# Kernel optimization log

Hardware: AMD Instinct MI355X
Metric: run time of the kernel (lower is better)

The kernel has to match this reference:

```python
import jax, jax.numpy as jnp
import numpy as np

B, L, D, H, NE, M, NP, C, F2 = 2, 1024, 768, 12, 42, 8, 1722, 97, 256


def setup_inputs() -> dict:
    key = jax.random.key(0)
    ks = jax.random.split(key, 12)
    s = 0.02
    sequence_output = jax.random.normal(ks[0], (B, L, D), jnp.float32)
    attention = jax.random.uniform(ks[1], (B, H, L, L), jnp.float32)
    mention_idx = jax.random.randint(ks[2], (B, NE, M), 0, L)
    mention_mask = jax.random.randint(ks[3], (B, NE, M), 0, 2).at[:, :, 0].set(1)
    hts = jax.random.randint(ks[4], (B, NP, 2), 0, NE)
    return dict(
        sequence_output=sequence_output, attention=attention,
        mention_idx=mention_idx, mention_mask=mention_mask, hts=hts,
        W_lin=jax.random.normal(ks[5], (D, 3)) * s, b_lin=jnp.zeros((3,)),
        W_seg=jax.random.normal(ks[6], (3, F2)) * s, b_seg=jnp.zeros((F2,)),
        W_head=jax.random.normal(ks[7], (D, F2)) * s, b_head=jnp.zeros((F2,)),
        W_tail=jax.random.normal(ks[8], (D, F2)) * s, b_tail=jnp.zeros((F2,)),
        W_bil=jax.random.normal(ks[9], (C, F2, F2)) * s, b_bil=jnp.zeros((C,)),
    )


def reference(sequence_output, attention, mention_idx, mention_mask, hts,
              W_lin, b_lin, W_seg, b_seg, W_head, b_head, W_tail, b_tail,
              W_bil, b_bil):
    b_, l_, d_ = sequence_output.shape
    h_ = attention.shape[1]
    ne, m_ = mention_idx.shape[1:]
    NEG = jnp.asarray(-1e30, sequence_output.dtype)
    msk = mention_mask.astype(sequence_output.dtype)  # [B,NE,M]

    bidx = jnp.arange(b_)[:, None, None]
    # --- get_hrt: per-entity mention gather + logsumexp pool / mean pool ---
    ment_emb = sequence_output[bidx, mention_idx]              # [B,NE,M,D]
    ent_emb = jax.nn.logsumexp(jnp.where(msk[..., None] > 0, ment_emb, NEG), axis=2)  # [B,NE,D]
    ment_att = attention[bidx, :, mention_idx]                 # [B,NE,M,H,L]
    ent_att = (ment_att * msk[..., None, None]).sum(2) / msk.sum(2)[..., None, None]  # [B,NE,H,L]

    b2 = jnp.arange(b_)[:, None]
    hs = ent_emb[b2, hts[..., 0]]                              # [B,NP,D]
    ts = ent_emb[b2, hts[..., 1]]

    # --- get_channel_map: all ne*ne pair attention-weighted context ---
    hi = jnp.repeat(jnp.arange(ne), ne)
    ti = jnp.tile(jnp.arange(ne), ne)
    h_att = ent_att[:, hi]                                     # [B,NE*NE,H,L]
    t_att = ent_att[:, ti]
    ht_att = jnp.einsum('bphl,bphl->bpl', h_att, t_att) / h_   # mean over heads
    ht_att = ht_att / (ht_att.sum(-1, keepdims=True) + 1e-5)
    rs = jnp.einsum('bld,bpl->bpd', sequence_output, ht_att)   # [B,NE*NE,D]
    feature_map = rs.reshape(b_, ne, ne, d_)

    # self.linear (D->3) then segmentation net (stand-in: 1x1 conv 3->F2 + relu)
    attn_input = feature_map @ W_lin + b_lin                   # [B,NE,NE,3]
    attn_map = jax.nn.relu(attn_input @ W_seg + b_seg)         # [B,NE,NE,F2]

    # --- get_ht: gather pair features ---
    h_t = attn_map[b2, hts[..., 0], hts[..., 1]]               # [B,NP,F2]
    hs = jnp.tanh(hs @ W_head + b_head + h_t)
    ts = jnp.tanh(ts @ W_tail + b_tail + h_t)
    logits = jnp.einsum('bpi,oij,bpj->bpo', hs, W_bil, ts) + b_bil
    return logits.reshape(-1, logits.shape[-1])               # [B*NP, C]
```

## Files before the change

kernel.cpp:

```cpp
#include <hip/hip_runtime.h>
#include <hip/hip_bf16.h>
#include <math.h>

constexpr int BB = 2;
constexpr int LL = 1024;
constexpr int DD = 768;
constexpr int HH = 12;
constexpr int NEz = 42;
constexpr int MM = 8;
constexpr int NPp = 1722;
constexpr int CC = 97;
constexpr int FF = 256;
constexpr int PAIRS = NEz * NEz;
constexpr int TOTAL = BB * NPp;
constexpr int MTv = 256;
constexpr int NTt = 14;
constexpr int PADR = 3584;
constexpr int NOGv = 36;
constexpr int NWGv = NTt * NOGv;

typedef float f32x4 __attribute__((ext_vector_type(4)));
typedef short bf16x8 __attribute__((ext_vector_type(8)));
typedef unsigned int u32x2 __attribute__((ext_vector_type(2)));

__device__ inline short f2bs(float x) {
    __hip_bfloat16 b = __float2bfloat16(x);
    return *(short*)&b;
}
__device__ inline void gload16(const void* g, void* l) {
    __builtin_amdgcn_global_load_lds((const __attribute__((address_space(1))) unsigned int*)g,
                                     (__attribute__((address_space(3))) unsigned int*)l, 16, 0, 0);
}

__global__ void k_ent_emb(const float* __restrict__ seq, const int* __restrict__ midx,
                          const int* __restrict__ mmask, float* __restrict__ ent_emb) {
    int be = blockIdx.x;
    int b = be / NEz;
    int tid = threadIdx.x;
    int idx[MM], msk[MM];
#pragma unroll
    for (int m = 0; m < MM; ++m) {
        idx[m] = midx[be * MM + m];
        msk[m] = mmask[be * MM + m];
    }
    const float* sb = seq + (size_t)b * LL * DD;
    for (int d = tid; d < DD; d += 256) {
        float v[MM];
        float mx = -1e30f;
#pragma unroll
        for (int m = 0; m < MM; ++m) {
            v[m] = msk[m] ? sb[(size_t)idx[m] * DD + d] : -1e30f;
            mx = fmaxf(mx, v[m]);
        }
        float s = 0.f;
#pragma unroll
        for (int m = 0; m < MM; ++m) s += expf(v[m] - mx);
        ent_emb[(size_t)be * DD + d] = mx + logf(s);
    }
}

__global__ void k_ent_att(const float* __restrict__ att, const int* __restrict__ midx,
                          const int* __restrict__ mmask, float* __restrict__ ea) {
    int beh = blockIdx.x;
    int h = beh % HH;
    int be = beh / HH;
    int b = be / NEz;
    int tid = threadIdx.x;
    int idx[MM], msk[MM];
    float msum = 0.f;
#pragma unroll
    for (int m = 0; m < MM; ++m) {
        idx[m] = midx[be * MM + m];
        msk[m] = mmask[be * MM + m];
        msum += (float)msk[m];
    }
    float inv = 1.f / msum;
    const float* ab = att + ((size_t)b * HH + h) * LL * LL;
#pragma unroll
    for (int li = 0; li < 4; ++li) {
        int l = tid + li * 256;
        float acc = 0.f;
#pragma unroll
        for (int m = 0; m < MM; ++m)
            if (msk[m]) acc += ab[(size_t)idx[m] * LL + l];
        ea[(size_t)beh * LL + l] = acc * inv;
    }
}

__global__ void k_pairAB(const float* __restrict__ ea, const float* __restrict__ seq,
                         const float* __restrict__ Wl, float* __restrict__ szp) {
    int lcb = blockIdx.x;
    int b = blockIdx.y;
    int l0 = lcb * 8;
    int tid = threadIdx.x;
    int lane = tid & 63;
    int e1 = (tid >> 6) * 8 + (lane >> 3);
    int l = lane & 7;

    __shared__ float S[NEz][HH][9];
    __shared__ float sw[8][3];
    __shared__ float swp[24][17];

    for (int idx = tid; idx < NEz * HH * 8; idx += 384) {
        int e = idx / 96, rem = idx % 96;
        int h = rem / 8, ll = rem % 8;
        S[e][h][ll] = ea[((size_t)(b * NEz + e) * HH + h) * LL + l0 + ll];
    }
    {
        int cpair = tid % 24, s = tid / 24;
        if (s < 16) {
            int ll = cpair / 3, kk = cpair % 3;
            const float* sr = seq + ((size_t)b * LL + l0 + ll) * DD;
            float p = 0.f;
            for (int d = s * 48; d < s * 48 + 48; ++d) p += sr[d] * Wl[d * 3 + kk];
            swp[cpair][s] = p;
        }
    }
    __syncthreads();
    if (tid < 24) {
        float s = 0.f;
#pragma unroll
        for (int i = 0; i < 16; ++i) s += swp[tid][i];
        sw[tid / 3][tid % 3] = s;
    }
    __syncthreads();

    bool act = e1 < NEz;
    float e1r[HH];
#pragma unroll
    for (int h = 0; h < HH; ++h) e1r[h] = act ? S[e1][h][l] : 0.f;
    float sw0 = sw[l][0], sw1 = sw[l][1], sw2 = sw[l][2];

    for (int e2 = 0; e2 < NEz; ++e2) {
        float ht = 0.f;
#pragma unroll
        for (int h = 0; h < HH; ++h) ht += e1r[h] * S[e2][h][l];
        ht *= (1.0f / HH);
        float v0 = ht, v1 = ht * sw0, v2 = ht * sw1, v3 = ht * sw2;
#pragma unroll
        for (int off = 1; off < 8; off <<= 1) {
            v0 += __shfl_xor(v0, off);
            v1 += __shfl_xor(v1, off);
            v2 += __shfl_xor(v2, off);
            v3 += __shfl_xor(v3, off);
        }
        if (act && l == 0) {
            float4 o4 = make_float4(v0, v1, v2, v3);
            *(float4*)&szp[(((size_t)(b * PAIRS + e1 * NEz + e2)) * 128 + lcb) * 4] = o4;
        }
    }
}

__global__ void k_zz(const float* __restrict__ szp, const float* __restrict__ blin,
                     float* __restrict__ zz) {
    int bp = blockIdx.x * 256 + threadIdx.x;
    if (bp >= BB * PAIRS) return;
    const float4* s = (const float4*)(szp + (size_t)bp * 512);
    float v0 = 0.f, v1 = 0.f, v2 = 0.f, v3 = 0.f;
#pragma unroll 8
    for (int i = 0; i < 128; ++i) {
        float4 a = s[i];
        v0 += a.x; v1 += a.y; v2 += a.z; v3 += a.w;
    }
    float inv = 1.f / (v0 + 1e-5f);
    float4 o4 = make_float4(v1 * inv + blin[0], v2 * inv + blin[1], v3 * inv + blin[2], 0.f);
    *(float4*)&zz[(size_t)bp * 4] = o4;
}

__global__ void k_ew(const float* __restrict__ ent_emb, const float* __restrict__ Wh,
                     const float* __restrict__ bh, const float* __restrict__ Wt,
                     const float* __restrict__ bt, float* __restrict__ EWh,
                     float* __restrict__ EWt) {
    int cb = blockIdx.x;
    int tid = threadIdx.x;
    int colg = cb * 8 + (tid & 7);
    int rg = tid >> 3;
    bool head = colg < FF;
    int col = head ? colg : colg - FF;
    const float* W = head ? Wh : Wt;
    float bias = head ? bh[col] : bt[col];
    float* dst = head ? EWh : EWt;
    for (int r = rg; r < BB * NEz; r += 32) {
        float s = bias;
        const float* e = ent_emb + (size_t)r * DD;
        for (int d = 0; d < DD; ++d) s += e[d] * W[(size_t)d * FF + col];
        dst[(size_t)r * FF + col] = s;
    }
}

__global__ void k_wt(const float* __restrict__ Wb, char* __restrict__ Wf) {
    int o = blockIdx.x >> 2, kc = blockIdx.x & 3;
    int tid = threadIdx.x;
    __shared__ float t64[64][257];
    const float* src = Wb + (size_t)o * FF * FF + (size_t)(kc * 64) * FF;
#pragma unroll
    for (int i = 0; i < 64; ++i) {
        int flat = i * 256 + tid;
        t64[flat >> 8][flat & 255] = src[flat];
    }
    __syncthreads();
    char* dst = Wf + ((size_t)o * 4 + kc) * 32768;
#pragma unroll
    for (int i = 0; i < 8; ++i) {
        int u = i * 256 + tid;
        int c = u >> 3, k16 = u & 7;
        bf16x8 v;
#pragma unroll
        for (int j = 0; j < 8; ++j) v[j] = f2bs(t64[k16 * 8 + j][c]);
        *(bf16x8*)(dst + ((c * 128 + k16 * 16) ^ ((c & 7) << 4))) = v;
    }
}

__global__ void k_prep(const float* __restrict__ EWh, const float* __restrict__ EWt,
                       const float* __restrict__ zz, const float* __restrict__ Wseg,
                       const float* __restrict__ bseg, const int* __restrict__ hts,
                       char* __restrict__ HSf, unsigned short* __restrict__ TSt) {
    int bx = blockIdx.x;
    int mt = bx >> 2, cs = bx & 3;
    int tid = threadIdx.x;
    int p0 = mt * MTv;

    __shared__ int offh[256], offt[256];
    __shared__ float zr[256][4];
    __shared__ float wsg[4][64];
    {
        int p = p0 + tid;
        if (p < TOTAL) {
            int b = p / NPp;
            int e1 = hts[p * 2], e2 = hts[p * 2 + 1];
            offh[tid] = (b * NEz + e1) * FF;
            offt[tid] = (b * NEz + e2) * FF;
            float4 z4 = *(const float4*)(zz + (size_t)(b * PAIRS + e1 * NEz + e2) * 4);
            zr[tid][0] = z4.x; zr[tid][1] = z4.y; zr[tid][2] = z4.z; zr[tid][3] = 0.f;
        } else {
            offh[tid] = -1; offt[tid] = -1;
            zr[tid][0] = zr[tid][1] = zr[tid][2] = zr[tid][3] = 0.f;
        }
        if (tid < 64) {
            int c = cs * 64 + tid;
            wsg[0][tid] = Wseg[c];
            wsg[1][tid] = Wseg[FF + c];
            wsg[2][tid] = Wseg[2 * FF + c];
            wsg[3][tid] = bseg[c];
        }
    }
    __syncthreads();

    char* dst = HSf + ((size_t)mt * 4 + cs) * 32768;
#pragma unroll
    for (int i = 0; i < 8; ++i) {
        int u = i * 256 + tid;
        int r = u >> 3, k8 = u & 7;
        int oh = offh[r];
        bf16x8 v = {0, 0, 0, 0, 0, 0, 0, 0};
        if (oh >= 0) {
#pragma unroll
            for (int j = 0; j < 8; ++j) {
                int cl = k8 * 8 + j;
                float ht = fmaxf(zr[r][0] * wsg[0][cl] + zr[r][1] * wsg[1][cl] +
                                 zr[r][2] * wsg[2][cl] + wsg[3][cl], 0.f);
                v[j] = f2bs(tanhf(EWh[oh + cs * 64 + cl] + ht));
            }
        }
        *(bf16x8*)(dst + ((r * 128 + k8 * 16) ^ ((r & 7) << 4))) = v;
    }
#pragma unroll
    for (int i = 0; i < 64; ++i) {
        int u = i * 256 + tid;
        int r = u & 255, cl = u >> 8;
        int c = cs * 64 + cl;
        int ot = offt[r];
        unsigned short v = 0;
        if (ot >= 0) {
            float ht = fmaxf(zr[r][0] * wsg[0][cl] + zr[r][1] * wsg[1][cl] +
                             zr[r][2] * wsg[2][cl] + wsg[3][cl], 0.f);
            v = (unsigned short)f2bs(tanhf(EWt[ot + c] + ht));
        }
        TSt[(size_t)c * PADR + p0 + r] = v;
    }
}

#define STAGE(TT, BUF) do { \
    int kc_ = (TT) & 3; \
    int o_ = og + NOGv * ((TT) >> 2); \
    const char* As_ = HSf + ((size_t)(mt * 4 + kc_)) * 32768; \
    const char* Bs_ = Wf + ((size_t)(o_ * 4 + kc_)) * 32768; \
    _Pragma("unroll") \
    for (int i_ = 0; i_ < 4; ++i_) { \
        gload16(As_ + (i_ * 512 + tid) * 16, Ab[BUF] + (i_ * 512 + tid) * 16); \
        gload16(Bs_ + (i_ * 512 + tid) * 16, Bb[BUF] + (i_ * 512 + tid) * 16); \
    } \
} while (0)

__launch_bounds__(512, 2)
__global__ void k_bil(const char* __restrict__ HSf, const unsigned short* __restrict__ TSt,
                      const char* __restrict__ Wf, const float* __restrict__ bbil,
                      float* __restrict__ out) {
    int f = blockIdx.x;
    int wg = (f & 7) * 63 + (f >> 3);
    int og = wg / NTt;
    int mt = wg % NTt;
    int p0 = mt * MTv;
    int nO = (og < 25) ? 3 : 2;

    int tid = threadIdx.x;
    int lane = tid & 63, w = tid >> 6;
    int wr = w >> 2, wc = w & 3;
    int lr = lane & 15, lg = lane >> 4;
    int swz = (lr & 7) << 4;

    __shared__ char Ab[2][32768];
    __shared__ char Bb[2][32768];
    __shared__ float red[MTv][4];

    STAGE(0, 0);
    STAGE(1, 1);

    f32x4 acc[8][4];
#pragma unroll
    for (int mi = 0; mi < 8; ++mi)
#pragma unroll
        for (int ni = 0; ni < 4; ++ni) acc[mi][ni] = (f32x4){0.f, 0.f, 0.f, 0.f};

    int T = 4 * nO;
    for (int t = 0; t < T; ++t) {
        int cur = t & 1;
        __builtin_amdgcn_sched_barrier(0);
        asm volatile("s_waitcnt vmcnt(8)" ::: "memory");
        __builtin_amdgcn_sched_barrier(0);
        __builtin_amdgcn_s_barrier();
        __builtin_amdgcn_sched_barrier(0);

        const char* Ac = Ab[cur];
        const char* Bc = Bb[cur];
        int kA = (lg * 16) ^ swz;
        int kB = (64 + lg * 16) ^ swz;

        bf16x8 a0[8], b0[4];
#pragma unroll
        for (int mi = 0; mi < 8; ++mi)
            a0[mi] = *(const bf16x8*)(Ac + (wr * 128 + mi * 16 + lr) * 128 + kA);
#pragma unroll
        for (int ni = 0; ni < 4; ++ni)
            b0[ni] = *(const bf16x8*)(Bc + (wc * 64 + ni * 16 + lr) * 128 + kA);
        __builtin_amdgcn_s_setprio(1);
#pragma unroll
        for (int mi = 0; mi < 8; ++mi)
#pragma unroll
            for (int ni = 0; ni < 4; ++ni)
                acc[mi][ni] = __builtin_amdgcn_mfma_f32_16x16x32_bf16(a0[mi], b0[ni], acc[mi][ni], 0, 0, 0);
        __builtin_amdgcn_s_setprio(0);

        bf16x8 a1[8], b1[4];
#pragma unroll
        for (int mi = 0; mi < 8; ++mi)
            a1[mi] = *(const bf16x8*)(Ac + (wr * 128 + mi * 16 + lr) * 128 + kB);
#pragma unroll
        for (int ni = 0; ni < 4; ++ni)
            b1[ni] = *(const bf16x8*)(Bc + (wc * 64 + ni * 16 + lr) * 128 + kB);
        __builtin_amdgcn_sched_barrier(0);
        asm volatile("s_waitcnt lgkmcnt(0)" ::: "memory");
        __builtin_amdgcn_sched_barrier(0);
        __builtin_amdgcn_s_barrier();
        __builtin_amdgcn_sched_barrier(0);

        int tt = (t + 2 < T) ? t + 2 : T - 1;
        STAGE(tt, cur);
        __builtin_amdgcn_sched_barrier(0);
        __builtin_amdgcn_s_setprio(1);
#pragma unroll
        for (int mi = 0; mi < 8; ++mi)
#pragma unroll
            for (int ni = 0; ni < 4; ++ni)
                acc[mi][ni] = __builtin_amdgcn_mfma_f32_16x16x32_bf16(a1[mi], b1[ni], acc[mi][ni], 0, 0, 0);
        __builtin_amdgcn_s_setprio(0);

        if ((t & 3) == 3) {
            int o = og + NOGv * (t >> 2);
            u32x2 tsv[8][4];
#pragma unroll
            for (int mi = 0; mi < 8; ++mi)
#pragma unroll
                for (int ni = 0; ni < 4; ++ni)
                    tsv[mi][ni] = *(const u32x2*)(TSt + (size_t)(wc * 64 + ni * 16 + lr) * PADR +
                                                  p0 + wr * 128 + mi * 16 + lg * 4);
#pragma unroll
            for (int mi = 0; mi < 8; ++mi) {
                float s0 = 0.f, s1 = 0.f, s2 = 0.f, s3 = 0.f;
#pragma unroll
                for (int ni = 0; ni < 4; ++ni) {
                    unsigned lo = tsv[mi][ni][0], hi = tsv[mi][ni][1];
                    s0 += acc[mi][ni][0] * __uint_as_float(lo << 16);
                    s1 += acc[mi][ni][1] * __uint_as_float(lo & 0xFFFF0000u);
                    s2 += acc[mi][ni][2] * __uint_as_float(hi << 16);
                    s3 += acc[mi][ni][3] * __uint_as_float(hi & 0xFFFF0000u);
                    acc[mi][ni] = (f32x4){0.f, 0.f, 0.f, 0.f};
                }
#pragma unroll
                for (int off = 1; off < 16; off <<= 1) {
                    s0 += __shfl_xor(s0, off);
                    s1 += __shfl_xor(s1, off);
                    s2 += __shfl_xor(s2, off);
                    s3 += __shfl_xor(s3, off);
                }
                if (lr == 0) {
                    int rb = wr * 128 + mi * 16 + lg * 4;
                    red[rb + 0][wc] = s0;
                    red[rb + 1][wc] = s1;
                    red[rb + 2][wc] = s2;
                    red[rb + 3][wc] = s3;
                }
            }
            __builtin_amdgcn_sched_barrier(0);
            asm volatile("s_waitcnt lgkmcnt(0)" ::: "memory");
            __builtin_amdgcn_sched_barrier(0);
            __builtin_amdgcn_s_barrier();
            __builtin_amdgcn_sched_barrier(0);
            if (tid < 256) {
                int p = p0 + tid;
                if (p < TOTAL)
                    out[(size_t)p * CC + o] =
                        red[tid][0] + red[tid][1] + red[tid][2] + red[tid][3] + bbil[o];
            }
        }
    }
}
#undef STAGE

extern "C" void kernel_launch(void* const* d_in, const int* in_sizes, int n_in,
                              void* d_out, int out_size, void* d_ws, size_t ws_size,
                              hipStream_t stream) {
    const float* seq   = (const float*)d_in[0];
    const float* att   = (const float*)d_in[1];
    const int*   midx  = (const int*)d_in[2];
    const int*   mmask = (const int*)d_in[3];
    const int*   hts   = (const int*)d_in[4];
    const float* Wlin  = (const float*)d_in[5];
    const float* blin  = (const float*)d_in[6];
    const float* Wseg  = (const float*)d_in[7];
    const float* bseg  = (const float*)d_in[8];
    const float* Whead = (const float*)d_in[9];
    const float* bhead = (const float*)d_in[10];
    const float* Wtail = (const float*)d_in[11];
    const float* btail = (const float*)d_in[12];
    const float* Wbil  = (const float*)d_in[13];
    const float* bbil  = (const float*)d_in[14];
    float* out = (float*)d_out;

    float* ws = (float*)d_ws;
    float* ent_emb = ws;
    float* ea      = ent_emb + BB * NEz * DD;
    float* szp     = ea + (size_t)BB * NEz * HH * LL;
    float* zz      = szp + (size_t)BB * PAIRS * 128 * 4;
    float* EWh     = zz + (size_t)BB * PAIRS * 4;
    float* EWt     = EWh + BB * NEz * FF;
    char* Wf       = (char*)(EWt + BB * NEz * FF);
    char* HSf      = Wf + (size_t)CC * 4 * 32768;
    unsigned short* TSt = (unsigned short*)(HSf + (size_t)NTt * 4 * 32768);

    k_ent_emb<<<BB * NEz, 256, 0, stream>>>(seq, midx, mmask, ent_emb);
    k_ent_att<<<BB * NEz * HH, 256, 0, stream>>>(att, midx, mmask, ea);
    k_pairAB<<<dim3(128, BB), 384, 0, stream>>>(ea, seq, Wlin, szp);
    k_zz<<<14, 256, 0, stream>>>(szp, blin, zz);
    k_ew<<<64, 256, 0, stream>>>(ent_emb, Whead, bhead, Wtail, btail, EWh, EWt);
    k_wt<<<CC * 4, 256, 0, stream>>>(Wbil, Wf);
    k_prep<<<NTt * 4, 256, 0, stream>>>(EWh, EWt, zz, Wseg, bseg, hts, HSf, TSt);
    k_bil<<<NWGv, 512, 0, stream>>>(HSf, TSt, Wf, bbil, out);
}
```

Before: 239.5 us.

## Halve bilinear M-tile, keep full A tile resident in LDS, parallelize zz reduction

The bilinear kernel now uses 128-row pair tiles, doubling the workgroup count to 1008. The full 128x256 bf16 head tile is loaded into LDS once per workgroup, so only W slices are streamed per k-chunk, and tail values are held in registers from the start. k_zz splits each pair's 128-element reduction across 8 lanes with shuffles. k_prep is restructured to stage tail embeddings through LDS with coalesced float4 loads. The cost is more LDS per block and smaller MFMA tiles per wave, which lowers arithmetic intensity per W load.

```diff
diff --git a/kernel.cpp b/kernel.cpp
--- a/kernel.cpp
+++ b/kernel.cpp
@@ -13,8 +13,8 @@
 constexpr int FF = 256;
 constexpr int PAIRS = NEz * NEz;
 constexpr int TOTAL = BB * NPp;
-constexpr int MTv = 256;
-constexpr int NTt = 14;
+constexpr int MTv = 128;
+constexpr int NTt = 28;
 constexpr int PADR = 3584;
 constexpr int NOGv = 36;
 constexpr int NWGv = NTt * NOGv;
@@ -153,18 +153,28 @@
 
 __global__ void k_zz(const float* __restrict__ szp, const float* __restrict__ blin,
                      float* __restrict__ zz) {
-    int bp = blockIdx.x * 256 + threadIdx.x;
+    int idx = blockIdx.x * 256 + threadIdx.x;
+    int bp = idx >> 3, s8 = idx & 7;
     if (bp >= BB * PAIRS) return;
-    const float4* s = (const float4*)(szp + (size_t)bp * 512);
+    const float4* s = (const float4*)(szp + (size_t)bp * 512) + s8 * 16;
     float v0 = 0.f, v1 = 0.f, v2 = 0.f, v3 = 0.f;
-#pragma unroll 8
-    for (int i = 0; i < 128; ++i) {
+#pragma unroll
+    for (int i = 0; i < 16; ++i) {
         float4 a = s[i];
         v0 += a.x; v1 += a.y; v2 += a.z; v3 += a.w;
     }
-    float inv = 1.f / (v0 + 1e-5f);
-    float4 o4 = make_float4(v1 * inv + blin[0], v2 * inv + blin[1], v3 * inv + blin[2], 0.f);
-    *(float4*)&zz[(size_t)bp * 4] = o4;
+#pragma unroll
+    for (int off = 1; off < 8; off <<= 1) {
+        v0 += __shfl_xor(v0, off);
+        v1 += __shfl_xor(v1, off);
+        v2 += __shfl_xor(v2, off);
+        v3 += __shfl_xor(v3, off);
+    }
+    if (s8 == 0) {
+        float inv = 1.f / (v0 + 1e-5f);
+        float4 o4 = make_float4(v1 * inv + blin[0], v2 * inv + blin[1], v3 * inv + blin[2], 0.f);
+        *(float4*)&zz[(size_t)bp * 4] = o4;
+    }
 }
 
 __global__ void k_ew(const float* __restrict__ ent_emb, const float* __restrict__ Wh,
@@ -215,81 +225,96 @@
                        const float* __restrict__ zz, const float* __restrict__ Wseg,
                        const float* __restrict__ bseg, const int* __restrict__ hts,
                        char* __restrict__ HSf, unsigned short* __restrict__ TSt) {
-    int bx = blockIdx.x;
-    int mt = bx >> 2, cs = bx & 3;
-    int tid = threadIdx.x;
-    int p0 = mt * MTv;
-
-    __shared__ int offh[256], offt[256];
-    __shared__ float zr[256][4];
-    __shared__ float wsg[4][64];
-    {
+    int tile = blockIdx.x >> 1, half = blockIdx.x & 1;
+    int tid = threadIdx.x;
+    int p0 = tile * MTv;
+
+    __shared__ int offh[128];
+    __shared__ float zr[128][3];
+    __shared__ float wsg[4][128];
+    __shared__ float Et[128][133];
+
+    if (tid < 128) {
         int p = p0 + tid;
         if (p < TOTAL) {
             int b = p / NPp;
             int e1 = hts[p * 2], e2 = hts[p * 2 + 1];
             offh[tid] = (b * NEz + e1) * FF;
-            offt[tid] = (b * NEz + e2) * FF;
             float4 z4 = *(const float4*)(zz + (size_t)(b * PAIRS + e1 * NEz + e2) * 4);
-            zr[tid][0] = z4.x; zr[tid][1] = z4.y; zr[tid][2] = z4.z; zr[tid][3] = 0.f;
+            zr[tid][0] = z4.x; zr[tid][1] = z4.y; zr[tid][2] = z4.z;
         } else {
-            offh[tid] = -1; offt[tid] = -1;
-            zr[tid][0] = zr[tid][1] = zr[tid][2] = zr[tid][3] = 0.f;
-        }
-        if (tid < 64) {
-            int c = cs * 64 + tid;
-            wsg[0][tid] = Wseg[c];
-            wsg[1][tid] = Wseg[FF + c];
-            wsg[2][tid] = Wseg[2 * FF + c];
-            wsg[3][tid] = bseg[c];
+            offh[tid] = -1;
+            zr[tid][0] = zr[tid][1] = zr[tid][2] = 0.f;
+        }
+        int c = half * 128 + tid;
+        wsg[0][tid] = Wseg[c];
+        wsg[1][tid] = Wseg[FF + c];
+        wsg[2][tid] = Wseg[2 * FF + c];
+        wsg[3][tid] = bseg[c];
+    }
+    {
+        int r2 = tid >> 1, hc = tid & 1;
+        int p = p0 + r2;
+        int ot = -1;
+        if (p < TOTAL) {
+            int b = p / NPp;
+            int e2 = hts[p * 2 + 1];
+            ot = (b * NEz + e2) * FF;
+        }
+#pragma unroll
+        for (int j = 0; j < 64; j += 4) {
+            float4 v = make_float4(0.f, 0.f, 0.f, 0.f);
+            if (ot >= 0) v = *(const float4*)(EWt + ot + half * 128 + hc * 64 + j);
+            int cl = hc * 64 + j;
+            Et[r2][cl] = v.x; Et[r2][cl + 1] = v.y; Et[r2][cl + 2] = v.z; Et[r2][cl + 3] = v.w;
         }
     }
     __syncthreads();
 
-    char* dst = HSf + ((size_t)mt * 4 + cs) * 32768;
+    char* dst = HSf + (size_t)tile * 65536;
 #pragma unroll
     for (int i = 0; i < 8; ++i) {
         int u = i * 256 + tid;
-        int r = u >> 3, k8 = u & 7;
+        int r = u >> 4, k16 = u & 15;
         int oh = offh[r];
         bf16x8 v = {0, 0, 0, 0, 0, 0, 0, 0};
         if (oh >= 0) {
 #pragma unroll
             for (int j = 0; j < 8; ++j) {
-                int cl = k8 * 8 + j;
+                int cl = k16 * 8 + j;
                 float ht = fmaxf(zr[r][0] * wsg[0][cl] + zr[r][1] * wsg[1][cl] +
                                  zr[r][2] * wsg[2][cl] + wsg[3][cl], 0.f);
-                v[j] = f2bs(tanhf(EWh[oh + cs * 64 + cl] + ht));
+                v[j] = f2bs(tanhf(EWh[oh + half * 128 + cl] + ht));
             }
         }
-        *(bf16x8*)(dst + ((r * 128 + k8 * 16) ^ ((r & 7) << 4))) = v;
-    }
-#pragma unroll
-    for (int i = 0; i < 64; ++i) {
-        int u = i * 256 + tid;
-        int r = u & 255, cl = u >> 8;
-        int c = cs * 64 + cl;
-        int ot = offt[r];
-        unsigned short v = 0;
-        if (ot >= 0) {
-            float ht = fmaxf(zr[r][0] * wsg[0][cl] + zr[r][1] * wsg[1][cl] +
-                             zr[r][2] * wsg[2][cl] + wsg[3][cl], 0.f);
-            v = (unsigned short)f2bs(tanhf(EWt[ot + c] + ht));
-        }
-        TSt[(size_t)c * PADR + p0 + r] = v;
-    }
-}
-
-#define STAGE(TT, BUF) do { \
-    int kc_ = (TT) & 3; \
-    int o_ = og + NOGv * ((TT) >> 2); \
-    const char* As_ = HSf + ((size_t)(mt * 4 + kc_)) * 32768; \
+        int byte = (r * 512 + half * 256 + k16 * 16) ^ ((r & 7) << 4);
+        *(bf16x8*)(dst + byte) = v;
+    }
+    {
+        int r = tid & 127, cg = tid >> 7;
+        int p = p0 + r;
+        bool act = p < TOTAL;
+        for (int i2 = 0; i2 < 64; ++i2) {
+            int cl = cg * 64 + i2;
+            unsigned short v = 0;
+            if (act) {
+                float ht = fmaxf(zr[r][0] * wsg[0][cl] + zr[r][1] * wsg[1][cl] +
+                                 zr[r][2] * wsg[2][cl] + wsg[3][cl], 0.f);
+                v = (unsigned short)f2bs(tanhf(Et[r][cl] + ht));
+            }
+            TSt[(size_t)(half * 128 + cl) * PADR + p0 + r] = v;
+        }
+    }
+}
+
+#define STAGE(C, BUF) do { \
+    int c_ = (C); \
+    int o_ = og + NOGv * (c_ >> 2); \
+    int kc_ = c_ & 3; \
     const char* Bs_ = Wf + ((size_t)(o_ * 4 + kc_)) * 32768; \
     _Pragma("unroll") \
-    for (int i_ = 0; i_ < 4; ++i_) { \
-        gload16(As_ + (i_ * 512 + tid) * 16, Ab[BUF] + (i_ * 512 + tid) * 16); \
+    for (int i_ = 0; i_ < 4; ++i_) \
         gload16(Bs_ + (i_ * 512 + tid) * 16, Bb[BUF] + (i_ * 512 + tid) * 16); \
-    } \
 } while (0)
 
 __launch_bounds__(512, 2)
@@ -297,7 +322,7 @@
                       const char* __restrict__ Wf, const float* __restrict__ bbil,
                       float* __restrict__ out) {
     int f = blockIdx.x;
-    int wg = (f & 7) * 63 + (f >> 3);
+    int wg = (f & 7) * 126 + (f >> 3);
     int og = wg / NTt;
     int mt = wg % NTt;
     int p0 = mt * MTv;
@@ -307,57 +332,81 @@
     int lane = tid & 63, w = tid >> 6;
     int wr = w >> 2, wc = w & 3;
     int lr = lane & 15, lg = lane >> 4;
-    int swz = (lr & 7) << 4;
-
-    __shared__ char Ab[2][32768];
+
+    __shared__ char A_l[65536];
     __shared__ char Bb[2][32768];
     __shared__ float red[MTv][4];
 
+    u32x2 tsv[4][4];
+#pragma unroll
+    for (int mi = 0; mi < 4; ++mi)
+#pragma unroll
+        for (int ni = 0; ni < 4; ++ni)
+            tsv[mi][ni] = *(const u32x2*)(TSt + (size_t)(wc * 64 + ni * 16 + lr) * PADR +
+                                          p0 + wr * 64 + mi * 16 + lg * 4);
+
+    {
+        const char* As = HSf + (size_t)mt * 65536;
+#pragma unroll
+        for (int i = 0; i < 8; ++i)
+            gload16(As + (i * 512 + tid) * 16, A_l + (i * 512 + tid) * 16);
+    }
     STAGE(0, 0);
     STAGE(1, 1);
 
-    f32x4 acc[8][4];
-#pragma unroll
-    for (int mi = 0; mi < 8; ++mi)
+    f32x4 acc[4][4];
+#pragma unroll
+    for (int mi = 0; mi < 4; ++mi)
 #pragma unroll
         for (int ni = 0; ni < 4; ++ni) acc[mi][ni] = (f32x4){0.f, 0.f, 0.f, 0.f};
 
     int T = 4 * nO;
     for (int t = 0; t < T; ++t) {
         int cur = t & 1;
-        __builtin_amdgcn_sched_barrier(0);
-        asm volatile("s_waitcnt vmcnt(8)" ::: "memory");
+        int kc = t & 3;
+        __builtin_amdgcn_sched_barrier(0);
+        asm volatile("s_waitcnt vmcnt(4)" ::: "memory");
         __builtin_amdgcn_sched_barrier(0);
         __builtin_amdgcn_s_barrier();
         __builtin_amdgcn_sched_barrier(0);
 
-        const char* Ac = Ab[cur];
         const char* Bc = Bb[cur];
-        int kA = (lg * 16) ^ swz;
-        int kB = (64 + lg * 16) ^ swz;
-
-        bf16x8 a0[8], b0[4];
-#pragma unroll
-        for (int mi = 0; mi < 8; ++mi)
-            a0[mi] = *(const bf16x8*)(Ac + (wr * 128 + mi * 16 + lr) * 128 + kA);
-#pragma unroll
-        for (int ni = 0; ni < 4; ++ni)
-            b0[ni] = *(const bf16x8*)(Bc + (wc * 64 + ni * 16 + lr) * 128 + kA);
+        int kA = kc * 128 + lg * 16;
+        int kB = kA + 64;
+
+        bf16x8 a0[4], b0[4];
+#pragma unroll
+        for (int mi = 0; mi < 4; ++mi) {
+            int r = wr * 64 + mi * 16 + lr;
+            a0[mi] = *(const bf16x8*)(A_l + ((r * 512 + kA) ^ ((r & 7) << 4)));
+        }
+#pragma unroll
+        for (int ni = 0; ni < 4; ++ni) {
+            int c = wc * 64 + ni * 16 + lr;
+            b0[ni] = *(const bf16x8*)(Bc + ((c * 128 + lg * 16) ^ ((c & 7) << 4)));
+        }
+        __builtin_amdgcn_sched_barrier(0);
+        asm volatile("s_waitcnt lgkmcnt(0)" ::: "memory");
+        __builtin_amdgcn_sched_barrier(0);
         __builtin_amdgcn_s_setprio(1);
 #pragma unroll
-        for (int mi = 0; mi < 8; ++mi)
+        for (int mi = 0; mi < 4; ++mi)
 #pragma unroll
             for (int ni = 0; ni < 4; ++ni)
                 acc[mi][ni] = __builtin_amdgcn_mfma_f32_16x16x32_bf16(a0[mi], b0[ni], acc[mi][ni], 0, 0, 0);
         __builtin_amdgcn_s_setprio(0);
 
-        bf16x8 a1[8], b1[4];
-#pragma unroll
-        for (int mi = 0; mi < 8; ++mi)
-            a1[mi] = *(const bf16x8*)(Ac + (wr * 128 + mi * 16 + lr) * 128 + kB);
-#pragma unroll
-        for (int ni = 0; ni < 4; ++ni)
-            b1[ni] = *(const bf16x8*)(Bc + (wc * 64 + ni * 16 + lr) * 128 + kB);
+        bf16x8 a1[4], b1[4];
+#pragma unroll
+        for (int mi = 0; mi < 4; ++mi) {
+            int r = wr * 64 + mi * 16 + lr;
+            a1[mi] = *(const bf16x8*)(A_l + ((r * 512 + kB) ^ ((r & 7) << 4)));
+        }
+#pragma unroll
+        for (int ni = 0; ni < 4; ++ni) {
+            int c = wc * 64 + ni * 16 + lr;
+            b1[ni] = *(const bf16x8*)(Bc + ((c * 128 + 64 + lg * 16) ^ ((c & 7) << 4)));
+        }
         __builtin_amdgcn_sched_barrier(0);
         asm volatile("s_waitcnt lgkmcnt(0)" ::: "memory");
         __builtin_amdgcn_sched_barrier(0);
@@ -369,7 +418,7 @@
         __builtin_amdgcn_sched_barrier(0);
         __builtin_amdgcn_s_setprio(1);
 #pragma unroll
-        for (int mi = 0; mi < 8; ++mi)
+        for (int mi = 0; mi < 4; ++mi)
 #pragma unroll
             for (int ni = 0; ni < 4; ++ni)
                 acc[mi][ni] = __builtin_amdgcn_mfma_f32_16x16x32_bf16(a1[mi], b1[ni], acc[mi][ni], 0, 0, 0);
@@ -377,15 +426,8 @@
 
         if ((t & 3) == 3) {
             int o = og + NOGv * (t >> 2);
-            u32x2 tsv[8][4];
-#pragma unroll
-            for (int mi = 0; mi < 8; ++mi)
-#pragma unroll
-                for (int ni = 0; ni < 4; ++ni)
-                    tsv[mi][ni] = *(const u32x2*)(TSt + (size_t)(wc * 64 + ni * 16 + lr) * PADR +
-                                                  p0 + wr * 128 + mi * 16 + lg * 4);
-#pragma unroll
-            for (int mi = 0; mi < 8; ++mi) {
+#pragma unroll
+            for (int mi = 0; mi < 4; ++mi) {
                 float s0 = 0.f, s1 = 0.f, s2 = 0.f, s3 = 0.f;
 #pragma unroll
                 for (int ni = 0; ni < 4; ++ni) {
@@ -404,7 +446,7 @@
                     s3 += __shfl_xor(s3, off);
                 }
                 if (lr == 0) {
-                    int rb = wr * 128 + mi * 16 + lg * 4;
+                    int rb = wr * 64 + mi * 16 + lg * 4;
                     red[rb + 0][wc] = s0;
                     red[rb + 1][wc] = s1;
                     red[rb + 2][wc] = s2;
@@ -416,7 +458,7 @@
             __builtin_amdgcn_sched_barrier(0);
             __builtin_amdgcn_s_barrier();
             __builtin_amdgcn_sched_barrier(0);
-            if (tid < 256) {
+            if (tid < MTv) {
                 int p = p0 + tid;
                 if (p < TOTAL)
                     out[(size_t)p * CC + o] =
@@ -456,14 +498,14 @@
     float* EWt     = EWh + BB * NEz * FF;
     char* Wf       = (char*)(EWt + BB * NEz * FF);
     char* HSf      = Wf + (size_t)CC * 4 * 32768;
-    unsigned short* TSt = (unsigned short*)(HSf + (size_t)NTt * 4 * 32768);
+    unsigned short* TSt = (unsigned short*)(HSf + (size_t)NTt * 65536);
 
     k_ent_emb<<<BB * NEz, 256, 0, stream>>>(seq, midx, mmask, ent_emb);
     k_ent_att<<<BB * NEz * HH, 256, 0, stream>>>(att, midx, mmask, ea);
     k_pairAB<<<dim3(128, BB), 384, 0, stream>>>(ea, seq, Wlin, szp);
-    k_zz<<<14, 256, 0, stream>>>(szp, blin, zz);
+    k_zz<<<(BB * PAIRS * 8 + 255) / 256, 256, 0, stream>>>(szp, blin, zz);
     k_ew<<<64, 256, 0, stream>>>(ent_emb, Whead, bhead, Wtail, btail, EWh, EWt);
     k_wt<<<CC * 4, 256, 0, stream>>>(Wbil, Wf);
-    k_prep<<<NTt * 4, 256, 0, stream>>>(EWh, EWt, zz, Wseg, bseg, hts, HSf, TSt);
+    k_prep<<<NTt * 2, 256, 0, stream>>>(EWh, EWt, zz, Wseg, bseg, hts, HSf, TSt);
     k_bil<<<NWGv, 512, 0, stream>>>(HSf, TSt, Wf, bbil, out);
 }
```

Result: faster. 219.8 us (-8.2%).
